# Performance work log

Hardware: AMD Instinct MI355X
Metric: run time of the kernel (lower is better)

The kernel has to match this reference:

```python
import jax, jax.numpy as jnp
import numpy as np

N = 163842        # icosphere level-6 vertex count
IN_F = 32
OUT_F = 32

def setup_inputs() -> dict:
    key = jax.random.key(0)
    k1, k2, k3, k4 = jax.random.split(key, 4)
    x = jax.random.normal(k1, (N, IN_F), dtype=jnp.float32)
    neigh_orders = jax.random.randint(k2, (7 * N,), 0, N, dtype=jnp.int64)
    # nn.Linear(7*in_features, out_features): W [out, 7*in], b [out]
    W = jax.random.normal(k3, (OUT_F, 7 * IN_F), dtype=jnp.float32) * (1.0 / np.sqrt(7 * IN_F))
    b = jax.random.normal(k4, (OUT_F,), dtype=jnp.float32) * 0.01
    return {"x": x, "neigh_orders": neigh_orders, "W": W, "b": b}

def reference(x, neigh_orders, W, b):
    # gather 7 neighbor rows per node, flatten to [N, 7*in], then linear
    mat = x[neigh_orders].reshape(x.shape[0], 7 * x.shape[1])  # [N, 7*in]
    return mat @ W.T + b  # [N, out]
```

## Files before the change

kernel.cpp:

```cpp
#include <hip/hip_runtime.h>

#define NNODES 163842
#define INF 32
#define OUTF 32
#define KTOT (7 * INF)
#define OPW 8

__global__ void transpose_W_kernel(const float* __restrict__ W,
                                   float* __restrict__ Wt) {
    int i = blockIdx.x * blockDim.x + threadIdx.x;
    if (i < KTOT * OUTF) {
        int k = i / OUTF;
        int o = i % OUTF;
        Wt[k * OUTF + o] = W[o * KTOT + k];
    }
}

__global__ __launch_bounds__(256) void onering_conv_split_kernel(
    const float* __restrict__ x,
    const int* __restrict__ idx,
    const float* __restrict__ Wt,
    const float* __restrict__ b,
    float* __restrict__ out) {
    int lane = threadIdx.x & 63;
    int og = __builtin_amdgcn_readfirstlane(threadIdx.x >> 6);
    int n = blockIdx.x * 64 + lane;
    bool valid = (n < NNODES);
    int nc = valid ? n : (NNODES - 1);

    int ib[7];
    int base = nc * 7;
#pragma unroll
    for (int j = 0; j < 7; ++j) ib[j] = idx[base + j];

    float acc[OPW];
#pragma unroll
    for (int o = 0; o < OPW; ++o) acc[o] = b[og * OPW + o];

    float4 buf0[8], buf1[8];
    {
        const float4* rp = (const float4*)(x + (size_t)ib[0] * INF);
#pragma unroll
        for (int q = 0; q < 8; ++q) buf0[q] = rp[q];
    }

#pragma unroll
    for (int j = 0; j < 7; ++j) {
        float4* curb = (j & 1) ? buf1 : buf0;
        float4* nxtb = (j & 1) ? buf0 : buf1;
        if (j < 6) {
            const float4* np = (const float4*)(x + (size_t)ib[j + 1] * INF);
#pragma unroll
            for (int q = 0; q < 8; ++q) nxtb[q] = np[q];
        }
        const float* xr = (const float*)curb;
#pragma unroll
        for (int f = 0; f < INF; ++f) {
            float xv = xr[f];
            const float* wrow = Wt + (j * INF + f) * OUTF + og * OPW;
#pragma unroll
            for (int o = 0; o < OPW; ++o) {
                acc[o] = fmaf(xv, wrow[o], acc[o]);
            }
        }
    }

    if (valid) {
        float4* op = (float4*)(out + (size_t)n * OUTF + og * OPW);
        op[0] = *((float4*)&acc[0]);
        op[1] = *((float4*)&acc[4]);
    }
}

extern "C" void kernel_launch(void* const* d_in, const int* in_sizes, int n_in,
                              void* d_out, int out_size, void* d_ws, size_t ws_size,
                              hipStream_t stream) {
    const float* x   = (const float*)d_in[0];
    const int*   idx = (const int*)d_in[1];
    const float* W   = (const float*)d_in[2];
    const float* b   = (const float*)d_in[3];
    float* out = (float*)d_out;
    float* Wt  = (float*)d_ws;

    transpose_W_kernel<<<(KTOT * OUTF + 255) / 256, 256, 0, stream>>>(W, Wt);

    int grid = (NNODES + 63) / 64;
    onering_conv_split_kernel<<<grid, 256, 0, stream>>>(x, idx, Wt, b, out);
}
```

Measured before the change: 149.4 us.

## Stage gathered neighbor rows in LDS via async global_load_lds with XOR swizzle

Replaces the per-thread register double-buffered gather, in which each of the four waves redundantly loaded all 7 neighbor rows, with a cooperative gather. Each block loads its 448 rows once into shared memory using direct global-to-LDS loads, and an XOR swizzle on the 16-byte chunks avoids bank conflicts on the later reads. The compute phase then reads rows from LDS, so the four output-group waves no longer each fetch the same gathered data from global memory. In exchange it uses 56KB of LDS per block, which limits occupancy and removes overlap between gather and compute inside a block.

```diff
diff --git a/kernel.cpp b/kernel.cpp
--- a/kernel.cpp
+++ b/kernel.cpp
@@ -5,6 +5,12 @@
 #define OUTF 32
 #define KTOT (7 * INF)
 #define OPW 8
+#define NPB 64
+#define ROWS (NPB * 7)
+#define CALLS (ROWS / 8)
+#define CPW (CALLS / 4)
+
+typedef unsigned int u32;
 
 __global__ void transpose_W_kernel(const float* __restrict__ W,
                                    float* __restrict__ Wt) {
@@ -16,57 +22,69 @@
     }
 }
 
-__global__ __launch_bounds__(256) void onering_conv_split_kernel(
+__global__ __launch_bounds__(256, 2) void onering_gather_lds_kernel(
     const float* __restrict__ x,
     const int* __restrict__ idx,
     const float* __restrict__ Wt,
     const float* __restrict__ b,
     float* __restrict__ out) {
-    int lane = threadIdx.x & 63;
-    int og = __builtin_amdgcn_readfirstlane(threadIdx.x >> 6);
-    int n = blockIdx.x * 64 + lane;
-    bool valid = (n < NNODES);
-    int nc = valid ? n : (NNODES - 1);
+    __shared__ float lds[ROWS * INF];
 
-    int ib[7];
-    int base = nc * 7;
+    const int tid  = threadIdx.x;
+    const int lane = tid & 63;
+    const int wq   = tid >> 6;
+    const int block0 = blockIdx.x * NPB;
+    const int base7  = block0 * 7;
+
+    const int lsub   = lane >> 3;
+    const int c_phys = lane & 7;
 #pragma unroll
-    for (int j = 0; j < 7; ++j) ib[j] = idx[base + j];
+    for (int qq = 0; qq < CPW; ++qq) {
+        int q = wq * CPW + qq;
+        int r = q * 8 + lsub;
+        int n = r / 7;
+        int c_data = c_phys ^ (n & 7);
+        int rowi = base7 + r;
+        rowi = min(rowi, 7 * NNODES - 1);
+        int xi = idx[rowi];
+        const float* gsrc = x + (size_t)xi * INF + c_data * 4;
+        float* ldst = lds + q * 256;
+        __builtin_amdgcn_global_load_lds(
+            (const __attribute__((address_space(1))) void*)gsrc,
+            (__attribute__((address_space(3))) void*)ldst,
+            16, 0, 0);
+    }
+    __syncthreads();
+
+    const int n  = lane;
+    const int g  = block0 + n;
+    const int nx = n & 7;
 
     float acc[OPW];
 #pragma unroll
-    for (int o = 0; o < OPW; ++o) acc[o] = b[og * OPW + o];
-
-    float4 buf0[8], buf1[8];
-    {
-        const float4* rp = (const float4*)(x + (size_t)ib[0] * INF);
-#pragma unroll
-        for (int q = 0; q < 8; ++q) buf0[q] = rp[q];
-    }
+    for (int o = 0; o < OPW; ++o) acc[o] = b[wq * OPW + o];
 
 #pragma unroll
     for (int j = 0; j < 7; ++j) {
-        float4* curb = (j & 1) ? buf1 : buf0;
-        float4* nxtb = (j & 1) ? buf0 : buf1;
-        if (j < 6) {
-            const float4* np = (const float4*)(x + (size_t)ib[j + 1] * INF);
+        const float* rowbase = lds + (n * 7 + j) * INF;
 #pragma unroll
-            for (int q = 0; q < 8; ++q) nxtb[q] = np[q];
-        }
-        const float* xr = (const float*)curb;
+        for (int c = 0; c < 8; ++c) {
+            int phys = c ^ nx;
+            float4 v = *(const float4*)(rowbase + phys * 4);
+            const float* w0 = Wt + (j * INF + c * 4) * OUTF + wq * OPW;
+            const float* vf = (const float*)&v;
 #pragma unroll
-        for (int f = 0; f < INF; ++f) {
-            float xv = xr[f];
-            const float* wrow = Wt + (j * INF + f) * OUTF + og * OPW;
+            for (int t = 0; t < 4; ++t) {
 #pragma unroll
-            for (int o = 0; o < OPW; ++o) {
-                acc[o] = fmaf(xv, wrow[o], acc[o]);
+                for (int o = 0; o < OPW; ++o) {
+                    acc[o] = fmaf(vf[t], w0[t * OUTF + o], acc[o]);
+                }
             }
         }
     }
 
-    if (valid) {
-        float4* op = (float4*)(out + (size_t)n * OUTF + og * OPW);
+    if (g < NNODES) {
+        float4* op = (float4*)(out + (size_t)g * OUTF + wq * OPW);
         op[0] = *((float4*)&acc[0]);
         op[1] = *((float4*)&acc[4]);
     }
@@ -84,6 +102,6 @@
 
     transpose_W_kernel<<<(KTOT * OUTF + 255) / 256, 256, 0, stream>>>(W, Wt);
 
-    int grid = (NNODES + 63) / 64;
-    onering_conv_split_kernel<<<grid, 256, 0, stream>>>(x, idx, Wt, b, out);
+    int grid = (NNODES + NPB - 1) / NPB;
+    onering_gather_lds_kernel<<<grid, 256, 0, stream>>>(x, idx, Wt, b, out);
 }
```

Result: slower. 253.8 us (+69.9%).

## Pipeline gathers by feature chunk across all seven neighbors with repacked weights

Applied to the files above, without the earlier changes.

The main kernel used to load each neighbor's full 32-float row in turn, double-buffered one neighbor ahead. It now loads one float4 chunk from all seven neighbors at once, double-buffering eight chunks, and the weight matrix is repacked so rows follow this chunk/neighbor order. The aim is more independent gather loads in flight per wave, with smaller buffers that may lower register pressure. The cost is that each wave touches seven rows at once with narrower per-row accesses, which could hurt cache-line use or coalescing.

```diff
diff --git a/kernel.cpp b/kernel.cpp
--- a/kernel.cpp
+++ b/kernel.cpp
@@ -6,61 +6,65 @@
 #define KTOT (7 * INF)
 #define OPW 8
 
-__global__ void transpose_W_kernel(const float* __restrict__ W,
-                                   float* __restrict__ Wt) {
+__global__ void repack_W_kernel(const float* __restrict__ W,
+                                float* __restrict__ Wt2) {
     int i = blockIdx.x * blockDim.x + threadIdx.x;
     if (i < KTOT * OUTF) {
-        int k = i / OUTF;
-        int o = i % OUTF;
-        Wt[k * OUTF + o] = W[o * KTOT + k];
+        int kk = i >> 5;
+        int oo = i & 31;
+        int j = kk >> 5;
+        int f = kk & 31;
+        int c = f >> 2;
+        int t = f & 3;
+        Wt2[(((c * 7 + j) << 2) + t) * 32 + oo] = W[oo * KTOT + kk];
     }
 }
 
-__global__ __launch_bounds__(256) void onering_conv_split_kernel(
+__global__ __launch_bounds__(256) void onering_chunk_kernel(
     const float* __restrict__ x,
     const int* __restrict__ idx,
-    const float* __restrict__ Wt,
+    const float* __restrict__ Wt2,
     const float* __restrict__ b,
     float* __restrict__ out) {
-    int lane = threadIdx.x & 63;
-    int og = __builtin_amdgcn_readfirstlane(threadIdx.x >> 6);
-    int n = blockIdx.x * 64 + lane;
-    bool valid = (n < NNODES);
-    int nc = valid ? n : (NNODES - 1);
+    const int lane = threadIdx.x & 63;
+    const int og = __builtin_amdgcn_readfirstlane(threadIdx.x >> 6);
+    const int n = blockIdx.x * 64 + lane;
+    const bool valid = (n < NNODES);
+    const int nc = valid ? n : (NNODES - 1);
 
-    int ib[7];
-    int base = nc * 7;
+    const int base = nc * 7;
+    const float* rp[7];
 #pragma unroll
-    for (int j = 0; j < 7; ++j) ib[j] = idx[base + j];
+    for (int j = 0; j < 7; ++j) rp[j] = x + (size_t)idx[base + j] * INF;
 
     float acc[OPW];
 #pragma unroll
     for (int o = 0; o < OPW; ++o) acc[o] = b[og * OPW + o];
 
-    float4 buf0[8], buf1[8];
-    {
-        const float4* rp = (const float4*)(x + (size_t)ib[0] * INF);
+    float4 bufA[7], bufB[7];
 #pragma unroll
-        for (int q = 0; q < 8; ++q) buf0[q] = rp[q];
-    }
+    for (int j = 0; j < 7; ++j) bufA[j] = *(const float4*)(rp[j]);
 
 #pragma unroll
-    for (int j = 0; j < 7; ++j) {
-        float4* curb = (j & 1) ? buf1 : buf0;
-        float4* nxtb = (j & 1) ? buf0 : buf1;
-        if (j < 6) {
-            const float4* np = (const float4*)(x + (size_t)ib[j + 1] * INF);
+    for (int c = 0; c < 8; ++c) {
+        float4* cur = (c & 1) ? bufB : bufA;
+        float4* nxt = (c & 1) ? bufA : bufB;
+        if (c < 7) {
 #pragma unroll
-            for (int q = 0; q < 8; ++q) nxtb[q] = np[q];
+            for (int j = 0; j < 7; ++j) {
+                nxt[j] = *(const float4*)(rp[j] + (c + 1) * 4);
+            }
         }
-        const float* xr = (const float*)curb;
 #pragma unroll
-        for (int f = 0; f < INF; ++f) {
-            float xv = xr[f];
-            const float* wrow = Wt + (j * INF + f) * OUTF + og * OPW;
+        for (int j = 0; j < 7; ++j) {
+            const float* vf = (const float*)&cur[j];
 #pragma unroll
-            for (int o = 0; o < OPW; ++o) {
-                acc[o] = fmaf(xv, wrow[o], acc[o]);
+            for (int t = 0; t < 4; ++t) {
+                const float* wrow = Wt2 + (((c * 7 + j) << 2) + t) * 32 + og * OPW;
+#pragma unroll
+                for (int o = 0; o < OPW; ++o) {
+                    acc[o] = fmaf(vf[t], wrow[o], acc[o]);
+                }
             }
         }
     }
@@ -80,10 +84,10 @@
     const float* W   = (const float*)d_in[2];
     const float* b   = (const float*)d_in[3];
     float* out = (float*)d_out;
-    float* Wt  = (float*)d_ws;
+    float* Wt2 = (float*)d_ws;
 
-    transpose_W_kernel<<<(KTOT * OUTF + 255) / 256, 256, 0, stream>>>(W, Wt);
+    repack_W_kernel<<<(KTOT * OUTF + 255) / 256, 256, 0, stream>>>(W, Wt2);
 
     int grid = (NNODES + 63) / 64;
-    onering_conv_split_kernel<<<grid, 256, 0, stream>>>(x, idx, Wt, b, out);
+    onering_chunk_kernel<<<grid, 256, 0, stream>>>(x, idx, Wt2, b, out);
 }
```

Measured after the change: 174.2 us. 16.6% more time.

## Stage gathered neighbor rows in swizzled LDS shared by four output-group waves

Applied to the files above, without the earlier changes.

Each block now loads its 448 neighbor indices and gathered x rows cooperatively into LDS with float4 loads, using an XOR swizzle to avoid bank conflicts. The four waves then read rows from LDS instead of each wave separately gathering the same rows from global memory. This removes the fourfold redundant global gathers and makes the loads more coalesced. The cost is 57KB of LDS per block, which limits occupancy, plus a barrier and scheduling hints.

```diff
diff --git a/kernel.cpp b/kernel.cpp
--- a/kernel.cpp
+++ b/kernel.cpp
@@ -3,8 +3,12 @@
 #define NNODES 163842
 #define INF 32
 #define OUTF 32
-#define KTOT (7 * INF)
+#define KTOT 224
 #define OPW 8
+#define NPB 64
+#define ROWS 448
+#define CHUNKS 3584
+#define KPT 14
 
 __global__ void transpose_W_kernel(const float* __restrict__ W,
                                    float* __restrict__ Wt) {
@@ -16,57 +20,76 @@
     }
 }
 
-__global__ __launch_bounds__(256) void onering_conv_split_kernel(
+__global__ __launch_bounds__(256, 2) void onering_smem_kernel(
     const float* __restrict__ x,
     const int* __restrict__ idx,
     const float* __restrict__ Wt,
     const float* __restrict__ b,
     float* __restrict__ out) {
-    int lane = threadIdx.x & 63;
-    int og = __builtin_amdgcn_readfirstlane(threadIdx.x >> 6);
-    int n = blockIdx.x * 64 + lane;
-    bool valid = (n < NNODES);
-    int nc = valid ? n : (NNODES - 1);
+    __shared__ float ldsx[ROWS * INF];
+    __shared__ int   lidx[ROWS];
 
-    int ib[7];
-    int base = nc * 7;
+    const int t = threadIdx.x;
+    const int block0 = blockIdx.x * NPB;
+    const int base7 = block0 * 7;
+
+    lidx[t] = idx[min(base7 + t, 7 * NNODES - 1)];
+    if (t < ROWS - 256) {
+        lidx[t + 256] = idx[min(base7 + t + 256, 7 * NNODES - 1)];
+    }
+    __syncthreads();
+
+    float4 v[KPT];
 #pragma unroll
-    for (int j = 0; j < 7; ++j) ib[j] = idx[base + j];
+    for (int k = 0; k < KPT; ++k) {
+        const int g = t + (k << 8);
+        const int r = g >> 3;
+        const int c = g & 7;
+        const int xi = lidx[r];
+        v[k] = *(const float4*)(x + (size_t)xi * INF + (c << 2));
+    }
+#pragma unroll
+    for (int k = 0; k < KPT; ++k) {
+        const int g = t + (k << 8);
+        const int r = g >> 3;
+        const int c = g & 7;
+        *(float4*)(ldsx + (r << 5) + (((c ^ (r & 7))) << 2)) = v[k];
+    }
+    __builtin_amdgcn_sched_group_barrier(0x100, KPT, 0);
+    __builtin_amdgcn_sched_group_barrier(0x020, KPT, 0);
+    __builtin_amdgcn_sched_group_barrier(0x200, KPT, 0);
+    __syncthreads();
+
+    const int lane = t & 63;
+    const int og = __builtin_amdgcn_readfirstlane(t >> 6);
+    const int n = lane;
+    const int g = block0 + n;
 
     float acc[OPW];
 #pragma unroll
     for (int o = 0; o < OPW; ++o) acc[o] = b[og * OPW + o];
 
-    float4 buf0[8], buf1[8];
-    {
-        const float4* rp = (const float4*)(x + (size_t)ib[0] * INF);
-#pragma unroll
-        for (int q = 0; q < 8; ++q) buf0[q] = rp[q];
-    }
-
 #pragma unroll
     for (int j = 0; j < 7; ++j) {
-        float4* curb = (j & 1) ? buf1 : buf0;
-        float4* nxtb = (j & 1) ? buf0 : buf1;
-        if (j < 6) {
-            const float4* np = (const float4*)(x + (size_t)ib[j + 1] * INF);
+        const int rn = n * 7 + j;
+        const float* rowb = ldsx + (rn << 5);
+        const int swz = rn & 7;
 #pragma unroll
-            for (int q = 0; q < 8; ++q) nxtb[q] = np[q];
-        }
-        const float* xr = (const float*)curb;
+        for (int c = 0; c < 8; ++c) {
+            float4 vv = *(const float4*)(rowb + ((c ^ swz) << 2));
+            const float* vf = (const float*)&vv;
 #pragma unroll
-        for (int f = 0; f < INF; ++f) {
-            float xv = xr[f];
-            const float* wrow = Wt + (j * INF + f) * OUTF + og * OPW;
+            for (int t4 = 0; t4 < 4; ++t4) {
+                const float* wrow = Wt + (((j << 5) + (c << 2) + t4) << 5) + og * OPW;
 #pragma unroll
-            for (int o = 0; o < OPW; ++o) {
-                acc[o] = fmaf(xv, wrow[o], acc[o]);
+                for (int o = 0; o < OPW; ++o)
+                    acc[o] = fmaf(vf[t4], wrow[o], acc[o]);
             }
         }
     }
 
-    if (valid) {
-        float4* op = (float4*)(out + (size_t)n * OUTF + og * OPW);
+    if (g < NNODES) {
+        float4* op = (float4*)(out + (size_t)g * OUTF + og * OPW);
         op[0] = *((float4*)&acc[0]);
         op[1] = *((float4*)&acc[4]);
     }
@@ -84,6 +107,6 @@
 
     transpose_W_kernel<<<(KTOT * OUTF + 255) / 256, 256, 0, stream>>>(W, Wt);
 
-    int grid = (NNODES + 63) / 64;
-    onering_conv_split_kernel<<<grid, 256, 0, stream>>>(x, idx, Wt, b, out);
+    int grid = (NNODES + NPB - 1) / NPB;
+    onering_smem_kernel<<<grid, 256, 0, stream>>>(x, idx, Wt, b, out);
 }
```

Result: slower. 201.6 us (+35.0%).
